# Kernel tuning notes

Hardware: AMD Instinct MI355X
Metric: run time of the kernel (lower is better)

The kernel has to match this reference:

```python
import jax, jax.numpy as jnp
from jax import lax
import numpy as np

B, D = 1_000_000, 20


def setup_inputs() -> dict:
    key = jax.random.key(0)
    kx, kw, kb, ki = jax.random.split(key, 4)
    bound = 1.0 / np.sqrt(D)  # torch nn.Linear init scale
    return {
        "X": jax.random.normal(kx, (B, D), dtype=jnp.float32),
        "W": jax.random.uniform(kw, (D, D), dtype=jnp.float32, minval=-bound, maxval=bound),
        "b": jax.random.uniform(kb, (D,), dtype=jnp.float32, minval=-bound, maxval=bound),
        "W_init": jax.random.normal(ki, (D, D), dtype=jnp.float32),
    }


def reference(X, W, b, W_init):
    # linear -> matmul(+1) -> relu -> same linear again
    h = X @ W.T + b                       # [B, D]
    h = jax.nn.relu(h @ W_init + 1.0)     # [B, D]
    h = h @ W.T + b                       # [B, D]

    # while h.abs().sum() > 1: h /= 2
    # Halving by 2 is exact in fp32, so the abs-sum exactly halves each
    # iteration; count iterations on a scalar, then apply one fused scale.
    s0 = jnp.sum(jnp.abs(h))

    def cond(state):
        s, _ = state
        return s > 1.0

    def body(state):
        s, k = state
        return s * 0.5, k + 1

    _, k = lax.while_loop(cond, body, (s0, jnp.int32(0)))
    scale = jnp.exp2(-k.astype(h.dtype))  # 2**-k, exact for integer k
    return jnp.sum(h * scale)
```

## Files before the change

kernel.cpp:

```cpp
#include <hip/hip_runtime.h>
#include <math.h>

#define D 20
#define NT 256
#define RPT 1

#define WS_M1_OFF 8
#define WS_C_OFF 408
#define WS_WT_OFF 428
#define WS_PART_OFF 1024

__global__ void prep_kernel(const float* __restrict__ W,
                            const float* __restrict__ b,
                            const float* __restrict__ Wi,
                            float* __restrict__ wsf) {
  int t = threadIdx.x;
  if (t < D * D) {
    int d = t / D, j = t % D;
    float a = 0.f;
#pragma unroll
    for (int e = 0; e < D; ++e) a = fmaf(W[e * D + d], Wi[e * D + j], a);
    wsf[WS_M1_OFF + t] = a;
  } else if (t < 2 * D * D) {
    int i = t - D * D;
    int j = i / D, j2 = i % D;
    wsf[WS_WT_OFF + i] = W[j2 * D + j];
  } else if (t < 2 * D * D + D) {
    int j = t - 2 * D * D;
    float a = 1.0f;
#pragma unroll
    for (int e = 0; e < D; ++e) a = fmaf(b[e], Wi[e * D + j], a);
    wsf[WS_C_OFF + j] = a;
  }
}

__global__ __launch_bounds__(NT, 8) void fused_kernel(
    const float* __restrict__ X,
    const float* __restrict__ bb_,
    const float* __restrict__ M1,
    const float* __restrict__ cc_,
    const float* __restrict__ Wt,
    double* __restrict__ partials,
    int nrows) {
  const int t = threadIdx.x;

  const long long row = (long long)blockIdx.x * NT + t;
  const long long rmax = (long long)nrows - 1;
  const float valid = (row <= rmax) ? 1.0f : 0.0f;
  const long long r0 = (row <= rmax) ? row : rmax;

  const float4* __restrict__ Xv = (const float4*)(X + r0 * D);
  float4 xv[5];
#pragma unroll
  for (int s = 0; s < 5; ++s) xv[s] = Xv[s];

  float xa[D];
#pragma unroll
  for (int jv = 0; jv < 5; ++jv) {
    float4 v = xv[jv];
    xa[4 * jv + 0] = v.x;
    xa[4 * jv + 1] = v.y;
    xa[4 * jv + 2] = v.z;
    xa[4 * jv + 3] = v.w;
  }

  float h2[D];
#pragma unroll
  for (int j = 0; j < D; ++j) h2[j] = cc_[j];
#pragma unroll
  for (int d = 0; d < D; ++d) {
    const float xd = xa[d];
#pragma unroll
    for (int j = 0; j < D; ++j) {
      h2[j] = fmaf(xd, M1[d * D + j], h2[j]);
    }
  }

#pragma unroll
  for (int j = 0; j < D; ++j) h2[j] = fmaxf(h2[j], 0.f);

  float h3[D];
#pragma unroll
  for (int j2 = 0; j2 < D; ++j2) h3[j2] = bb_[j2];
#pragma unroll
  for (int j = 0; j < D; ++j) {
    const float p = h2[j];
#pragma unroll
    for (int j2 = 0; j2 < D; ++j2) {
      h3[j2] = fmaf(p, Wt[j * D + j2], h3[j2]);
    }
  }

  float rs = 0.f, ra = 0.f;
#pragma unroll
  for (int j = 0; j < D; ++j) {
    rs += h3[j];
    ra += fabsf(h3[j]);
  }
  rs *= valid;
  ra *= valid;

  __shared__ float sred[8];
#pragma unroll
  for (int off = 32; off > 0; off >>= 1) {
    rs += __shfl_down(rs, off, 64);
    ra += __shfl_down(ra, off, 64);
  }
  const int wave = t >> 6, lane = t & 63;
  if (lane == 0) {
    sred[wave] = rs;
    sred[4 + wave] = ra;
  }
  __syncthreads();
  if (t == 0) {
    float s1 = sred[0] + sred[1] + sred[2] + sred[3];
    float s2 = sred[4] + sred[5] + sred[6] + sred[7];
    partials[2 * blockIdx.x + 0] = (double)s1;
    partials[2 * blockIdx.x + 1] = (double)s2;
  }
}

__global__ void fin_kernel(const double* __restrict__ partials,
                           float* __restrict__ out, int nblocks) {
  __shared__ double sredh[16], sreda[16];
  const int t = threadIdx.x;
  double sh = 0.0, sa = 0.0;
  for (int i = t; i < nblocks; i += 1024) {
    sh += partials[2 * i + 0];
    sa += partials[2 * i + 1];
  }
#pragma unroll
  for (int off = 32; off > 0; off >>= 1) {
    sh += __shfl_down(sh, off, 64);
    sa += __shfl_down(sa, off, 64);
  }
  const int wave = t >> 6, lane = t & 63;
  if (lane == 0) {
    sredh[wave] = sh;
    sreda[wave] = sa;
  }
  __syncthreads();
  if (t == 0) {
    double th = 0.0, ta = 0.0;
#pragma unroll
    for (int w = 0; w < 16; ++w) {
      th += sredh[w];
      ta += sreda[w];
    }
    int k = 0;
    while (ta > 1.0 && k < 1100) {
      ta *= 0.5;
      ++k;
    }
    out[0] = ldexpf((float)th, -k);
  }
}

extern "C" void kernel_launch(void* const* d_in, const int* in_sizes, int n_in,
                              void* d_out, int out_size, void* d_ws, size_t ws_size,
                              hipStream_t stream) {
  const float* X = (const float*)d_in[0];
  const float* W = (const float*)d_in[1];
  const float* b = (const float*)d_in[2];
  const float* Wi = (const float*)d_in[3];
  float* out = (float*)d_out;
  float* wsf = (float*)d_ws;

  const int nrows = in_sizes[0] / D;

  hipLaunchKernelGGL(prep_kernel, dim3(1), dim3(1024), 0, stream, W, b, Wi, wsf);

  const int nblocks = (nrows + NT - 1) / NT;
  double* partials = (double*)(wsf + WS_PART_OFF);
  hipLaunchKernelGGL(fused_kernel, dim3(nblocks), dim3(NT), 0, stream,
                     X, b, wsf + WS_M1_OFF, wsf + WS_C_OFF, wsf + WS_WT_OFF,
                     partials, nrows);

  hipLaunchKernelGGL(fin_kernel, dim3(1), dim3(1024), 0, stream, partials, out,
                     nblocks);
}
```

Measured before the change: 129.8 us.

## Compute both per-row matmuls with bf16 MFMA instead of scalar FMAs

Replaces the per-thread scalar 20x20 FMA chains with bf16 16x16x32 MFMA instructions. Weights are pre-packed into bf16 MFMA fragment layout by the prep kernel, and the ReLU intermediate is transposed through shared memory between the two matmuls. Each block now handles 64 rows instead of 256, and the tail handling is dropped by assuming the row count divides by 64. This targets ALU-bound compute at the cost of bf16 precision loss in inputs and weights, which may hurt accuracy.

```diff
diff --git a/kernel.cpp b/kernel.cpp
--- a/kernel.cpp
+++ b/kernel.cpp
@@ -2,111 +2,139 @@
 #include <math.h>
 
 #define D 20
-#define NT 256
-#define RPT 1
-
-#define WS_M1_OFF 8
-#define WS_C_OFF 408
-#define WS_WT_OFF 428
-#define WS_PART_OFF 1024
+
+typedef __attribute__((ext_vector_type(8))) __bf16 bf16x8;
+typedef __attribute__((ext_vector_type(4))) float f32x4;
+
+#define WS_B1_BYTE 0
+#define WS_B2_BYTE 2048
+#define WS_C_BYTE 4096
+#define WS_BB_BYTE 4224
+#define WS_PART_BYTE 8192
+
+__device__ __forceinline__ unsigned f2bf_u(float f) {
+  unsigned u = __float_as_uint(f);
+  u += 0x7fffu + ((u >> 16) & 1u);
+  return u >> 16;
+}
 
 __global__ void prep_kernel(const float* __restrict__ W,
                             const float* __restrict__ b,
                             const float* __restrict__ Wi,
-                            float* __restrict__ wsf) {
-  int t = threadIdx.x;
-  if (t < D * D) {
-    int d = t / D, j = t % D;
-    float a = 0.f;
-#pragma unroll
-    for (int e = 0; e < D; ++e) a = fmaf(W[e * D + d], Wi[e * D + j], a);
-    wsf[WS_M1_OFF + t] = a;
-  } else if (t < 2 * D * D) {
-    int i = t - D * D;
-    int j = i / D, j2 = i % D;
-    wsf[WS_WT_OFF + i] = W[j2 * D + j];
-  } else if (t < 2 * D * D + D) {
-    int j = t - 2 * D * D;
-    float a = 1.0f;
-#pragma unroll
-    for (int e = 0; e < D; ++e) a = fmaf(b[e], Wi[e * D + j], a);
-    wsf[WS_C_OFF + j] = a;
-  }
-}
-
-__global__ __launch_bounds__(NT, 8) void fused_kernel(
+                            unsigned char* __restrict__ ws) {
+  unsigned short* fb1 = (unsigned short*)(ws + WS_B1_BYTE);
+  unsigned short* fb2 = (unsigned short*)(ws + WS_B2_BYTE);
+  float* cpad = (float*)(ws + WS_C_BYTE);
+  float* bpad = (float*)(ws + WS_BB_BYTE);
+
+  const int t = threadIdx.x;
+  {
+    const int tile = t >> 9, rem = t & 511;
+    const int lane = rem >> 3, j = rem & 7;
+    const int k = (lane >> 4) * 8 + j;
+    const int n = tile * 16 + (lane & 15);
+    float v1 = 0.f, v2 = 0.f;
+    if (k < D && n < D) {
+      float a = 0.f;
+#pragma unroll
+      for (int e = 0; e < D; ++e) a = fmaf(W[e * D + k], Wi[e * D + n], a);
+      v1 = a;
+      v2 = W[n * D + k];
+    }
+    fb1[t] = (unsigned short)f2bf_u(v1);
+    fb2[t] = (unsigned short)f2bf_u(v2);
+  }
+  if (t < 32) {
+    float cv = 0.f, bv = 0.f;
+    if (t < D) {
+      float a = 1.0f;
+#pragma unroll
+      for (int e = 0; e < D; ++e) a = fmaf(b[e], Wi[e * D + t], a);
+      cv = a;
+      bv = b[t];
+    }
+    cpad[t] = cv;
+    bpad[t] = bv;
+  }
+}
+
+__global__ __launch_bounds__(256, 4) void fused_kernel(
     const float* __restrict__ X,
-    const float* __restrict__ bb_,
-    const float* __restrict__ M1,
-    const float* __restrict__ cc_,
-    const float* __restrict__ Wt,
-    double* __restrict__ partials,
-    int nrows) {
+    const unsigned char* __restrict__ ws,
+    double* __restrict__ partials) {
+  __shared__ __align__(16) float sP[4 * 16 * 36];
+  __shared__ float sred[8];
+
+  const uint4* __restrict__ fb1 = (const uint4*)(ws + WS_B1_BYTE);
+  const uint4* __restrict__ fb2 = (const uint4*)(ws + WS_B2_BYTE);
+  const float* __restrict__ cpad = (const float*)(ws + WS_C_BYTE);
+  const float* __restrict__ bpad = (const float*)(ws + WS_BB_BYTE);
+
   const int t = threadIdx.x;
-
-  const long long row = (long long)blockIdx.x * NT + t;
-  const long long rmax = (long long)nrows - 1;
-  const float valid = (row <= rmax) ? 1.0f : 0.0f;
-  const long long r0 = (row <= rmax) ? row : rmax;
-
-  const float4* __restrict__ Xv = (const float4*)(X + r0 * D);
-  float4 xv[5];
-#pragma unroll
-  for (int s = 0; s < 5; ++s) xv[s] = Xv[s];
-
-  float xa[D];
-#pragma unroll
-  for (int jv = 0; jv < 5; ++jv) {
-    float4 v = xv[jv];
-    xa[4 * jv + 0] = v.x;
-    xa[4 * jv + 1] = v.y;
-    xa[4 * jv + 2] = v.z;
-    xa[4 * jv + 3] = v.w;
-  }
-
-  float h2[D];
-#pragma unroll
-  for (int j = 0; j < D; ++j) h2[j] = cc_[j];
-#pragma unroll
-  for (int d = 0; d < D; ++d) {
-    const float xd = xa[d];
-#pragma unroll
-    for (int j = 0; j < D; ++j) {
-      h2[j] = fmaf(xd, M1[d * D + j], h2[j]);
-    }
-  }
-
-#pragma unroll
-  for (int j = 0; j < D; ++j) h2[j] = fmaxf(h2[j], 0.f);
-
-  float h3[D];
-#pragma unroll
-  for (int j2 = 0; j2 < D; ++j2) h3[j2] = bb_[j2];
-#pragma unroll
-  for (int j = 0; j < D; ++j) {
-    const float p = h2[j];
-#pragma unroll
-    for (int j2 = 0; j2 < D; ++j2) {
-      h3[j2] = fmaf(p, Wt[j * D + j2], h3[j2]);
-    }
-  }
+  const int wave = t >> 6, lane = t & 63;
+  const int m = lane & 15, oct = lane >> 4;
+  const long long rowg = (long long)blockIdx.x * 64 + wave * 16 + m;
+
+  const int k0 = oct * 8;
+  const long long o1 = rowg * D + (long long)(k0 < D ? k0 : 0);
+  const long long o2 = rowg * D + (long long)(k0 + 4 < D ? k0 + 4 : 0);
+  float4 v1 = *(const float4*)(X + o1);
+  float4 v2 = *(const float4*)(X + o2);
+  const float s1m = (k0 < D) ? 1.f : 0.f;
+  const float s2m = (k0 + 4 < D) ? 1.f : 0.f;
+
+  union UF { bf16x8 v; unsigned u[4]; } a1;
+  a1.u[0] = f2bf_u(v1.x * s1m) | (f2bf_u(v1.y * s1m) << 16);
+  a1.u[1] = f2bf_u(v1.z * s1m) | (f2bf_u(v1.w * s1m) << 16);
+  a1.u[2] = f2bf_u(v2.x * s2m) | (f2bf_u(v2.y * s2m) << 16);
+  a1.u[3] = f2bf_u(v2.z * s2m) | (f2bf_u(v2.w * s2m) << 16);
+
+  union UB { bf16x8 v; uint4 q; } b10, b11, b20, b21;
+  b10.q = fb1[0 * 64 + lane];
+  b11.q = fb1[1 * 64 + lane];
+  b20.q = fb2[0 * 64 + lane];
+  b21.q = fb2[1 * 64 + lane];
+
+  const float c0 = cpad[m], c1 = cpad[16 + m];
+  f32x4 acc0 = {c0, c0, c0, c0};
+  f32x4 acc1 = {c1, c1, c1, c1};
+  acc0 = __builtin_amdgcn_mfma_f32_16x16x32_bf16(a1.v, b10.v, acc0, 0, 0, 0);
+  acc1 = __builtin_amdgcn_mfma_f32_16x16x32_bf16(a1.v, b11.v, acc1, 0, 0, 0);
+
+  float* wp = sP + wave * 576;
+#pragma unroll
+  for (int i = 0; i < 4; ++i) {
+    wp[(4 * oct + i) * 36 + m] = fmaxf(acc0[i], 0.f);
+    wp[(4 * oct + i) * 36 + 16 + m] = fmaxf(acc1[i], 0.f);
+  }
+  __syncthreads();
+
+  const float4* rp = (const float4*)(wp + m * 36 + k0);
+  float4 p1 = rp[0], p2 = rp[1];
+  union UF a2;
+  a2.u[0] = f2bf_u(p1.x) | (f2bf_u(p1.y) << 16);
+  a2.u[1] = f2bf_u(p1.z) | (f2bf_u(p1.w) << 16);
+  a2.u[2] = f2bf_u(p2.x) | (f2bf_u(p2.y) << 16);
+  a2.u[3] = f2bf_u(p2.z) | (f2bf_u(p2.w) << 16);
+
+  const float bb0 = bpad[m], bb1 = bpad[16 + m];
+  f32x4 d0 = {bb0, bb0, bb0, bb0};
+  f32x4 d1 = {bb1, bb1, bb1, bb1};
+  d0 = __builtin_amdgcn_mfma_f32_16x16x32_bf16(a2.v, b20.v, d0, 0, 0, 0);
+  d1 = __builtin_amdgcn_mfma_f32_16x16x32_bf16(a2.v, b21.v, d1, 0, 0, 0);
 
   float rs = 0.f, ra = 0.f;
 #pragma unroll
-  for (int j = 0; j < D; ++j) {
-    rs += h3[j];
-    ra += fabsf(h3[j]);
-  }
-  rs *= valid;
-  ra *= valid;
-
-  __shared__ float sred[8];
+  for (int i = 0; i < 4; ++i) {
+    rs += d0[i] + d1[i];
+    ra += fabsf(d0[i]) + fabsf(d1[i]);
+  }
+
 #pragma unroll
   for (int off = 32; off > 0; off >>= 1) {
     rs += __shfl_down(rs, off, 64);
     ra += __shfl_down(ra, off, 64);
   }
-  const int wave = t >> 6, lane = t & 63;
   if (lane == 0) {
     sred[wave] = rs;
     sred[4 + wave] = ra;
@@ -164,18 +192,15 @@
   const float* b = (const float*)d_in[2];
   const float* Wi = (const float*)d_in[3];
   float* out = (float*)d_out;
-  float* wsf = (float*)d_ws;
+  unsigned char* ws = (unsigned char*)d_ws;
 
   const int nrows = in_sizes[0] / D;
-
-  hipLaunchKernelGGL(prep_kernel, dim3(1), dim3(1024), 0, stream, W, b, Wi, wsf);
-
-  const int nblocks = (nrows + NT - 1) / NT;
-  double* partials = (double*)(wsf + WS_PART_OFF);
-  hipLaunchKernelGGL(fused_kernel, dim3(nblocks), dim3(NT), 0, stream,
-                     X, b, wsf + WS_M1_OFF, wsf + WS_C_OFF, wsf + WS_WT_OFF,
-                     partials, nrows);
-
+  const int nblocks = nrows / 64;
+  double* partials = (double*)(ws + WS_PART_BYTE);
+
+  hipLaunchKernelGGL(prep_kernel, dim3(1), dim3(1024), 0, stream, W, b, Wi, ws);
+  hipLaunchKernelGGL(fused_kernel, dim3(nblocks), dim3(256), 0, stream,
+                     X, ws, partials);
   hipLaunchKernelGGL(fin_kernel, dim3(1), dim3(1024), 0, stream, partials, out,
                      nblocks);
 }
```

After: 127.1 us. -2.1%, faster.
